# Optimization experiments

Measured on AMD Instinct MI355X. Metric: run time of the kernel, lower is better.

Reference implementation:

```python
import jax, jax.numpy as jnp
import numpy as np

# Dimensions: input_capsules=output_capsules=2048, slot_size=64, capsule_size=256
# slots_per_core = ceil(256/64) = 4, patch_size = (8,8) so h*w == slot_size
CI, CO, SLOT, SPC, H, W = 2048, 2048, 64, 4, 8, 8
PROBA = 0.1   # connection_probability
EPS = 1e-6    # flax nnx.LayerNorm default epsilon


def setup_inputs() -> dict:
    key = jax.random.key(0)
    k1, k2, k3 = jax.random.split(key, 3)
    x = jax.random.normal(k1, (CI, SPC, H, W), jnp.float32)
    # Wi: glorot_normal as in nnx initializers.glorot_normal()
    Wi = jax.nn.initializers.glorot_normal()(k2, (CI, SLOT, SLOT, SPC, SPC), jnp.float32)
    # LayerNorm params over the fully-flattened vector (input_capsules*capsule_size)
    ln_scale = jnp.ones((CI * SPC * SLOT,), jnp.float32)
    ln_bias = jnp.zeros((CI * SPC * SLOT,), jnp.float32)
    # Co: random sparse binary routing tensor (fast_scrramble), Bernoulli(proba)
    Co = jax.random.bernoulli(k3, PROBA, (CI, SPC, CO, SPC)).astype(jnp.float32)
    return {"x": x, "Wi": Wi, "ln_scale": ln_scale, "ln_bias": ln_bias, "Co": Co}


def reference(x, Wi, ln_scale, ln_bias, Co):
    ci, p, h, w = x.shape
    xr = x.reshape(ci, p, h * w)                      # 'ci p1 h w -> ci p1 (h w)'
    # per-capsule block matmul: 'ijklm, imk -> ilj'
    y = jnp.einsum('ijklm,imk->ilj', Wi, xr)          # (ci, spc, slot)
    y = jax.nn.gelu(y)                                # nnx.gelu (approximate tanh)
    shp = y.shape
    yf = y.reshape(-1)
    mu = jnp.mean(yf)
    var = jnp.var(yf)
    yf = (yf - mu) * jax.lax.rsqrt(var + EPS) * ln_scale + ln_bias  # global LayerNorm
    y = yf.reshape(shp)
    # sparse random-routing mixing: 'ijkl, ijm -> klm'
    out = jnp.einsum('ijkl,ijm->klm', Co, y)          # (co, spc, slot)
    return out.reshape(out.shape[0], out.shape[1], h, w)
```

## Files before the change

kernel.cpp:

```cpp
#include <hip/hip_runtime.h>
#include <hip/hip_bf16.h>

#define CI 2048
#define CO_N 2048
#define SLOT 64
#define SPC 4
#define NELEM (CI*SPC*SLOT)
#define CAP 256
#define IJ (CI*SPC)
#define S_SPLIT 8
#define NC 32

typedef __attribute__((ext_vector_type(8))) short short8;
typedef __attribute__((ext_vector_type(4))) short short4v;
typedef __attribute__((ext_vector_type(4))) float float4v;

union ABFrag { short4v h[2]; short8 v; };

__device__ __forceinline__ unsigned short f2bf(float f) {
    __hip_bfloat16 h = __float2bfloat16(f);
    return __builtin_bit_cast(unsigned short, h);
}

__device__ __forceinline__ float gelu_tanh(float x) {
    const float c0 = 0.7978845608028654f;
    float x3 = x * x * x;
    float t = tanhf(c0 * (x + 0.044715f * x3));
    return 0.5f * x * (1.0f + t);
}

__global__ __launch_bounds__(256) void k1_capsule_mm(
    const float* __restrict__ x, const float* __restrict__ Wi,
    float* __restrict__ y, float* __restrict__ psum, float* __restrict__ psumsq)
{
    __shared__ float xs[CAP];
    __shared__ float ws_s[4], ws_q[4];
    const int i = blockIdx.x;
    const int t = threadIdx.x;
    {
        const int m = t >> 6, k = t & 63;
        xs[k * 4 + m] = x[(size_t)i * CAP + t];
    }
    __syncthreads();

    const int j = t >> 2;
    const int l = t & 3;
    const float* Wb = Wi + (size_t)i * 65536 + j * 1024 + l * 4;
    float p = 0.f;
    #pragma unroll 8
    for (int k = 0; k < 64; ++k) {
        float4 wv = *(const float4*)(Wb + k * 16);
        float4 xv = *(const float4*)(xs + k * 4);
        p += wv.x * xv.x + wv.y * xv.y + wv.z * xv.z + wv.w * xv.w;
    }
    float g = gelu_tanh(p);
    y[(size_t)i * CAP + l * 64 + j] = g;

    float s = g, q = g * g;
    #pragma unroll
    for (int off = 32; off > 0; off >>= 1) {
        s += __shfl_down(s, off);
        q += __shfl_down(q, off);
    }
    const int w = t >> 6;
    if ((t & 63) == 0) { ws_s[w] = s; ws_q[w] = q; }
    __syncthreads();
    if (t == 0) {
        psum[i]   = ws_s[0] + ws_s[1] + ws_s[2] + ws_s[3];
        psumsq[i] = ws_q[0] + ws_q[1] + ws_q[2] + ws_q[3];
    }
}

__global__ __launch_bounds__(256) void k3_norm_t(
    const float* __restrict__ y, const float* __restrict__ scale,
    const float* __restrict__ bias, const float* __restrict__ psum,
    const float* __restrict__ psumsq, unsigned short* __restrict__ ynT)
{
    __shared__ float as[4], aq[4];
    __shared__ float sh_mu, sh_inv;
    const int c = blockIdx.x;
    const int t = threadIdx.x;

    float s = 0.f, q = 0.f;
    #pragma unroll
    for (int b = t; b < CI; b += 256) { s += psum[b]; q += psumsq[b]; }
    #pragma unroll
    for (int off = 32; off > 0; off >>= 1) {
        s += __shfl_down(s, off);
        q += __shfl_down(q, off);
    }
    if ((t & 63) == 0) { as[t >> 6] = s; aq[t >> 6] = q; }
    __syncthreads();
    if (t == 0) {
        float S = as[0] + as[1] + as[2] + as[3];
        float Q = aq[0] + aq[1] + aq[2] + aq[3];
        float mu = S / (float)NELEM;
        float var = Q / (float)NELEM - mu * mu;
        sh_mu = mu;
        sh_inv = rsqrtf(var + 1e-6f);
    }
    __syncthreads();
    const float mu = sh_mu, inv = sh_inv;

    const int base = c * 2048 + t * 8;
    float4 ya = *(const float4*)(y + base);
    float4 yb = *(const float4*)(y + base + 4);
    float4 sa = *(const float4*)(scale + base);
    float4 sb = *(const float4*)(scale + base + 4);
    float4 ba = *(const float4*)(bias + base);
    float4 bb = *(const float4*)(bias + base + 4);
    const int ij = c * 32 + (t >> 3);
    const int m0 = (t & 7) * 8;
    float v[8] = { (ya.x-mu)*inv*sa.x+ba.x, (ya.y-mu)*inv*sa.y+ba.y,
                   (ya.z-mu)*inv*sa.z+ba.z, (ya.w-mu)*inv*sa.w+ba.w,
                   (yb.x-mu)*inv*sb.x+bb.x, (yb.y-mu)*inv*sb.y+bb.y,
                   (yb.z-mu)*inv*sb.z+bb.z, (yb.w-mu)*inv*sb.w+bb.w };
    #pragma unroll
    for (int e = 0; e < 8; ++e)
        ynT[(size_t)(m0 + e) * IJ + ij] = f2bf(v[e]);
}

__global__ __launch_bounds__(256) void k4_route_mfma(
    const float* __restrict__ Co, const unsigned short* __restrict__ ynT,
    float* __restrict__ out, float* __restrict__ partial, int use_partial)
{
    __shared__ unsigned short lds_a[2][64 * 36];
    const int t    = threadIdx.x;
    const int kb   = blockIdx.x;
    const int pc   = blockIdx.y;
    const int klb  = kb * 64;
    const int w    = t >> 6;
    const int lane = t & 63;
    const int quad = lane >> 4;
    const int n16  = lane & 15;

    const int p  = t >> 4;
    const int c4 = (t & 15) * 4;

    const float* co_base = Co + ((size_t)(pc * 1024 + 2 * p)) * IJ + klb + c4;
    const unsigned short* ynT_base = ynT + (size_t)(pc * 1024) + quad * 8;

    float4v acc[4];
    #pragma unroll
    for (int mt = 0; mt < 4; ++mt) acc[mt] = (float4v)(0.f);

    float4 co0 = *(const float4*)(co_base);
    float4 co1 = *(const float4*)(co_base + IJ);
    short8 bcur[4], bnxt[4];
    #pragma unroll
    for (int mt = 0; mt < 4; ++mt)
        bcur[mt] = *(const short8*)(ynT_base + (size_t)(mt * 16 + n16) * IJ);

    for (int g = 0; g < NC; ++g) {
        unsigned int* lw = (unsigned int*)lds_a[g & 1];
        lw[(c4 + 0) * 18 + p] = (unsigned int)f2bf(co0.x) | ((unsigned int)f2bf(co1.x) << 16);
        lw[(c4 + 1) * 18 + p] = (unsigned int)f2bf(co0.y) | ((unsigned int)f2bf(co1.y) << 16);
        lw[(c4 + 2) * 18 + p] = (unsigned int)f2bf(co0.z) | ((unsigned int)f2bf(co1.z) << 16);
        lw[(c4 + 3) * 18 + p] = (unsigned int)f2bf(co0.w) | ((unsigned int)f2bf(co1.w) << 16);
        __syncthreads();

        if (g + 1 < NC) {
            const float* nb = co_base + (size_t)(g + 1) * 32 * IJ;
            co0 = *(const float4*)(nb);
            co1 = *(const float4*)(nb + IJ);
            const unsigned short* yb = ynT_base + (size_t)(g + 1) * 32;
            #pragma unroll
            for (int mt = 0; mt < 4; ++mt)
                bnxt[mt] = *(const short8*)(yb + (size_t)(mt * 16 + n16) * IJ);
        }

        const unsigned short* arow = lds_a[g & 1] + (w * 16 + n16) * 36 + quad * 8;
        ABFrag af;
        af.h[0] = *(const short4v*)(arow);
        af.h[1] = *(const short4v*)(arow + 4);
        #pragma unroll
        for (int mt = 0; mt < 4; ++mt)
            acc[mt] = __builtin_amdgcn_mfma_f32_16x16x32_bf16(af.v, bcur[mt], acc[mt], 0, 0, 0);

        if (g + 1 < NC) {
            #pragma unroll
            for (int mt = 0; mt < 4; ++mt) bcur[mt] = bnxt[mt];
        }
    }

    if (use_partial) {
        float* pp = partial + (size_t)pc * NELEM;
        #pragma unroll
        for (int mt = 0; mt < 4; ++mt)
            #pragma unroll
            for (int r = 0; r < 4; ++r)
                pp[(size_t)(klb + w * 16 + quad * 4 + r) * 64 + mt * 16 + n16] = acc[mt][r];
    } else {
        #pragma unroll
        for (int mt = 0; mt < 4; ++mt)
            #pragma unroll
            for (int r = 0; r < 4; ++r)
                atomicAdd(out + (size_t)(klb + w * 16 + quad * 4 + r) * 64 + mt * 16 + n16, acc[mt][r]);
    }
}

__global__ __launch_bounds__(256) void k5_reduce(
    const float* __restrict__ partial, float* __restrict__ out)
{
    const int idx = blockIdx.x * 256 + threadIdx.x;
    float s = 0.f;
    #pragma unroll
    for (int pcs = 0; pcs < S_SPLIT; ++pcs) s += partial[(size_t)pcs * NELEM + idx];
    out[idx] = s;
}

extern "C" void kernel_launch(void* const* d_in, const int* in_sizes, int n_in,
                              void* d_out, int out_size, void* d_ws, size_t ws_size,
                              hipStream_t stream) {
    const float* x        = (const float*)d_in[0];
    const float* Wi       = (const float*)d_in[1];
    const float* ln_scale = (const float*)d_in[2];
    const float* ln_bias  = (const float*)d_in[3];
    const float* Co       = (const float*)d_in[4];
    float* out = (float*)d_out;

    float* ws = (float*)d_ws;
    float* y      = ws;
    float* psum   = y + NELEM;
    float* psumsq = psum + CI;
    unsigned short* ynT = (unsigned short*)(ws + 528392);
    float* partial = ws + 790536;

    const int use_partial = (ws_size >= (size_t)(790536 + S_SPLIT * NELEM) * sizeof(float)) ? 1 : 0;

    k1_capsule_mm<<<CI, 256, 0, stream>>>(x, Wi, y, psum, psumsq);
    k3_norm_t<<<256, 256, 0, stream>>>(y, ln_scale, ln_bias, psum, psumsq, ynT);
    if (!use_partial)
        hipMemsetAsync(out, 0, (size_t)out_size * sizeof(float), stream);
    k4_route_mfma<<<dim3(128, S_SPLIT), 256, 0, stream>>>(Co, ynT, out, partial, use_partial);
    if (use_partial)
        k5_reduce<<<NELEM / 256, 256, 0, stream>>>(partial, out);
}
```

Baseline: 873.0 us.

## Fuse all stages into one cooperative kernel with grid-wide syncs

Replaces the four-to-five separate launches (capsule matmul, norm/transpose, routing MFMA, reduce) with a single cooperative kernel of 1024 blocks. Grid syncs separate the stages, and each block handles two capsules in the first stage. This removes per-launch overhead and inter-kernel gaps. In exchange it depends on cooperative launch support and on all blocks being co-resident, which launch_bounds(256,4) is meant to allow, and grid.sync itself has a cost. The old multi-kernel path stays as a fallback if the cooperative launch fails.

Result: slower. 1.253 ms (+43.5%).

```diff
diff --git a/kernel.cpp b/kernel.cpp
--- a/kernel.cpp
+++ b/kernel.cpp
@@ -1,5 +1,8 @@
 #include <hip/hip_runtime.h>
 #include <hip/hip_bf16.h>
+#include <hip/hip_cooperative_groups.h>
+
+namespace cg = cooperative_groups;
 
 #define CI 2048
 #define CO_N 2048
@@ -27,6 +30,183 @@
     float x3 = x * x * x;
     float t = tanhf(c0 * (x + 0.044715f * x3));
     return 0.5f * x * (1.0f + t);
+}
+
+__global__ __launch_bounds__(256, 4) void fused_all(
+    const float* __restrict__ x, const float* __restrict__ Wi,
+    const float* __restrict__ scale, const float* __restrict__ bias,
+    const float* __restrict__ Co, float* __restrict__ out,
+    float* __restrict__ y, float* __restrict__ psum, float* __restrict__ psumsq,
+    unsigned short* __restrict__ ynT, float* __restrict__ partial, int use_partial)
+{
+    __shared__ float xs[CAP];
+    __shared__ float red_s[4], red_q[4];
+    __shared__ float sh_mu, sh_inv;
+    __shared__ unsigned short lds_a[2][64 * 36];
+
+    const int t  = threadIdx.x;
+    const int bx = blockIdx.x;
+    cg::grid_group grid = cg::this_grid();
+
+    #pragma unroll 1
+    for (int cc = 0; cc < 2; ++cc) {
+        const int i = bx * 2 + cc;
+        {
+            const int m = t >> 6, k = t & 63;
+            xs[k * 4 + m] = x[(size_t)i * CAP + t];
+        }
+        __syncthreads();
+        const int j = t >> 2;
+        const int l = t & 3;
+        const float* Wb = Wi + (size_t)i * 65536 + j * 1024 + l * 4;
+        float p = 0.f;
+        #pragma unroll 8
+        for (int k = 0; k < 64; ++k) {
+            float4 wv = *(const float4*)(Wb + k * 16);
+            float4 xv = *(const float4*)(xs + k * 4);
+            p += wv.x * xv.x + wv.y * xv.y + wv.z * xv.z + wv.w * xv.w;
+        }
+        float g = gelu_tanh(p);
+        y[(size_t)i * CAP + l * 64 + j] = g;
+
+        float s = g, q = g * g;
+        #pragma unroll
+        for (int off = 32; off > 0; off >>= 1) {
+            s += __shfl_down(s, off);
+            q += __shfl_down(q, off);
+        }
+        if ((t & 63) == 0) { red_s[t >> 6] = s; red_q[t >> 6] = q; }
+        __syncthreads();
+        if (t == 0) {
+            psum[i]   = red_s[0] + red_s[1] + red_s[2] + red_s[3];
+            psumsq[i] = red_q[0] + red_q[1] + red_q[2] + red_q[3];
+        }
+        __syncthreads();
+    }
+
+    grid.sync();
+
+    {
+        float s = 0.f, q = 0.f;
+        #pragma unroll
+        for (int b = t; b < CI; b += 256) { s += psum[b]; q += psumsq[b]; }
+        #pragma unroll
+        for (int off = 32; off > 0; off >>= 1) {
+            s += __shfl_down(s, off);
+            q += __shfl_down(q, off);
+        }
+        if ((t & 63) == 0) { red_s[t >> 6] = s; red_q[t >> 6] = q; }
+        __syncthreads();
+        if (t == 0) {
+            float S = red_s[0] + red_s[1] + red_s[2] + red_s[3];
+            float Q = red_q[0] + red_q[1] + red_q[2] + red_q[3];
+            float mu = S / (float)NELEM;
+            float var = Q / (float)NELEM - mu * mu;
+            sh_mu  = mu;
+            sh_inv = rsqrtf(var + 1e-6f);
+        }
+        __syncthreads();
+        const float mu = sh_mu, inv = sh_inv;
+
+        const int idx = bx * 512 + t * 2;
+        float2 yv = *(const float2*)(y + idx);
+        float2 sv = *(const float2*)(scale + idx);
+        float2 bv = *(const float2*)(bias + idx);
+        const int ij = idx >> 6;
+        const int m  = idx & 63;
+        ynT[(size_t)m       * IJ + ij] = f2bf((yv.x - mu) * inv * sv.x + bv.x);
+        ynT[(size_t)(m + 1) * IJ + ij] = f2bf((yv.y - mu) * inv * sv.y + bv.y);
+        if (!use_partial) {
+            *(float2*)(out + idx) = make_float2(0.f, 0.f);
+        }
+    }
+
+    grid.sync();
+
+    {
+        const int kb   = bx & 127;
+        const int pc   = bx >> 7;
+        const int klb  = kb * 64;
+        const int w    = t >> 6;
+        const int lane = t & 63;
+        const int quad = lane >> 4;
+        const int n16  = lane & 15;
+        const int p    = t >> 4;
+        const int c4   = (t & 15) * 4;
+
+        const float* co_base = Co + ((size_t)(pc * 1024 + 2 * p)) * IJ + klb + c4;
+        const unsigned short* ynT_base = ynT + (size_t)(pc * 1024) + quad * 8;
+
+        float4v acc[4];
+        #pragma unroll
+        for (int mt = 0; mt < 4; ++mt) acc[mt] = (float4v)(0.f);
+
+        float4 co0 = *(const float4*)(co_base);
+        float4 co1 = *(const float4*)(co_base + IJ);
+        short8 bcur[4], bnxt[4];
+        #pragma unroll
+        for (int mt = 0; mt < 4; ++mt)
+            bcur[mt] = *(const short8*)(ynT_base + (size_t)(mt * 16 + n16) * IJ);
+
+        for (int g = 0; g < NC; ++g) {
+            unsigned int* lw = (unsigned int*)lds_a[g & 1];
+            lw[(c4 + 0) * 18 + p] = (unsigned int)f2bf(co0.x) | ((unsigned int)f2bf(co1.x) << 16);
+            lw[(c4 + 1) * 18 + p] = (unsigned int)f2bf(co0.y) | ((unsigned int)f2bf(co1.y) << 16);
+            lw[(c4 + 2) * 18 + p] = (unsigned int)f2bf(co0.z) | ((unsigned int)f2bf(co1.z) << 16);
+            lw[(c4 + 3) * 18 + p] = (unsigned int)f2bf(co0.w) | ((unsigned int)f2bf(co1.w) << 16);
+            __syncthreads();
+
+            if (g + 1 < NC) {
+                const float* nb = co_base + (size_t)(g + 1) * 32 * IJ;
+                co0 = *(const float4*)(nb);
+                co1 = *(const float4*)(nb + IJ);
+                const unsigned short* yb = ynT_base + (size_t)(g + 1) * 32;
+                #pragma unroll
+                for (int mt = 0; mt < 4; ++mt)
+                    bnxt[mt] = *(const short8*)(yb + (size_t)(mt * 16 + n16) * IJ);
+            }
+
+            const unsigned short* arow = lds_a[g & 1] + (w * 16 + n16) * 36 + quad * 8;
+            ABFrag af;
+            af.h[0] = *(const short4v*)(arow);
+            af.h[1] = *(const short4v*)(arow + 4);
+            #pragma unroll
+            for (int mt = 0; mt < 4; ++mt)
+                acc[mt] = __builtin_amdgcn_mfma_f32_16x16x32_bf16(af.v, bcur[mt], acc[mt], 0, 0, 0);
+
+            if (g + 1 < NC) {
+                #pragma unroll
+                for (int mt = 0; mt < 4; ++mt) bcur[mt] = bnxt[mt];
+            }
+        }
+
+        if (use_partial) {
+            float* pp = partial + (size_t)pc * NELEM;
+            #pragma unroll
+            for (int mt = 0; mt < 4; ++mt)
+                #pragma unroll
+                for (int r = 0; r < 4; ++r)
+                    pp[(size_t)(klb + w * 16 + quad * 4 + r) * 64 + mt * 16 + n16] = acc[mt][r];
+        } else {
+            #pragma unroll
+            for (int mt = 0; mt < 4; ++mt)
+                #pragma unroll
+                for (int r = 0; r < 4; ++r)
+                    atomicAdd(out + (size_t)(klb + w * 16 + quad * 4 + r) * 64 + mt * 16 + n16, acc[mt][r]);
+        }
+    }
+
+    if (use_partial) {
+        grid.sync();
+        const int idx = bx * 512 + t * 2;
+        float sx = 0.f, sy = 0.f;
+        #pragma unroll
+        for (int pcs = 0; pcs < S_SPLIT; ++pcs) {
+            float2 v = *(const float2*)(partial + (size_t)pcs * NELEM + idx);
+            sx += v.x; sy += v.y;
+        }
+        *(float2*)(out + idx) = make_float2(sx, sy);
+    }
 }
 
 __global__ __launch_bounds__(256) void k1_capsule_mm(
@@ -42,9 +222,7 @@
         xs[k * 4 + m] = x[(size_t)i * CAP + t];
     }
     __syncthreads();
-
-    const int j = t >> 2;
-    const int l = t & 3;
+    const int j = t >> 2, l = t & 3;
     const float* Wb = Wi + (size_t)i * 65536 + j * 1024 + l * 4;
     float p = 0.f;
     #pragma unroll 8
@@ -55,7 +233,6 @@
     }
     float g = gelu_tanh(p);
     y[(size_t)i * CAP + l * 64 + j] = g;
-
     float s = g, q = g * g;
     #pragma unroll
     for (int off = 32; off > 0; off >>= 1) {
@@ -80,7 +257,6 @@
     __shared__ float sh_mu, sh_inv;
     const int c = blockIdx.x;
     const int t = threadIdx.x;
-
     float s = 0.f, q = 0.f;
     #pragma unroll
     for (int b = t; b < CI; b += 256) { s += psum[b]; q += psumsq[b]; }
@@ -101,7 +277,6 @@
     }
     __syncthreads();
     const float mu = sh_mu, inv = sh_inv;
-
     const int base = c * 2048 + t * 8;
     float4 ya = *(const float4*)(y + base);
     float4 yb = *(const float4*)(y + base + 4);
@@ -133,7 +308,6 @@
     const int lane = t & 63;
     const int quad = lane >> 4;
     const int n16  = lane & 15;
-
     const int p  = t >> 4;
     const int c4 = (t & 15) * 4;
 
@@ -226,13 +400,20 @@
     unsigned short* ynT = (unsigned short*)(ws + 528392);
     float* partial = ws + 790536;
 
-    const int use_partial = (ws_size >= (size_t)(790536 + S_SPLIT * NELEM) * sizeof(float)) ? 1 : 0;
-
-    k1_capsule_mm<<<CI, 256, 0, stream>>>(x, Wi, y, psum, psumsq);
-    k3_norm_t<<<256, 256, 0, stream>>>(y, ln_scale, ln_bias, psum, psumsq, ynT);
-    if (!use_partial)
-        hipMemsetAsync(out, 0, (size_t)out_size * sizeof(float), stream);
-    k4_route_mfma<<<dim3(128, S_SPLIT), 256, 0, stream>>>(Co, ynT, out, partial, use_partial);
-    if (use_partial)
-        k5_reduce<<<NELEM / 256, 256, 0, stream>>>(partial, out);
-}
+    int use_partial = (ws_size >= (size_t)(790536 + S_SPLIT * NELEM) * sizeof(float)) ? 1 : 0;
+
+    void* args[] = { (void*)&x, (void*)&Wi, (void*)&ln_scale, (void*)&ln_bias,
+                     (void*)&Co, (void*)&out, (void*)&y, (void*)&psum,
+                     (void*)&psumsq, (void*)&ynT, (void*)&partial, (void*)&use_partial };
+    hipError_t err = hipLaunchCooperativeKernel((const void*)fused_all,
+                                                dim3(1024), dim3(256), args, 0, stream);
+    if (err != hipSuccess) {
+        k1_capsule_mm<<<CI, 256, 0, stream>>>(x, Wi, y, psum, psumsq);
+        k3_norm_t<<<256, 256, 0, stream>>>(y, ln_scale, ln_bias, psum, psumsq, ynT);
+        if (!use_partial)
+            hipMemsetAsync(out, 0, (size_t)out_size * sizeof(float), stream);
+        k4_route_mfma<<<dim3(128, S_SPLIT), 256, 0, stream>>>(Co, ynT, out, partial, use_partial);
+        if (use_partial)
+            k5_reduce<<<NELEM / 256, 256, 0, stream>>>(partial, out);
+    }
+}
```
